# Performance work log

Measured on AMD Instinct MI355X. Metric: run time of the kernel, lower is better.

Reference implementation:

```python
import jax, jax.numpy as jnp
import numpy as np

N = 32768      # total nodes
E = 262144     # total edges
B = 32         # graphs in batch
NP = N // B    # nodes per graph (equal-sized graphs)
K = 820        # ceil(0.8 * NP), PyG TopKPooling k
H, C = 8, 64   # heads, per-head channels
NEG_SLOPE = 0.2


def setup_inputs() -> dict:
    key = jax.random.key(0)
    ks = jax.random.split(key, 12)
    s = 0.05
    return {
        "x": jax.random.normal(ks[0], (N, 256), jnp.float32),
        "edge_attr": jax.random.normal(ks[1], (E, 32), jnp.float32),
        "Wl": jax.random.normal(ks[2], (256, H * C), jnp.float32) * s,
        "bl": jax.random.normal(ks[3], (H * C,), jnp.float32) * s,
        "Wr": jax.random.normal(ks[4], (256, H * C), jnp.float32) * s,
        "br": jax.random.normal(ks[5], (H * C,), jnp.float32) * s,
        "We": jax.random.normal(ks[6], (32, H * C), jnp.float32) * s,
        "att": jax.random.normal(ks[7], (H, C), jnp.float32) * s,
        "bias": jax.random.normal(ks[8], (H * C,), jnp.float32) * s,
        "pool_w": jax.random.normal(ks[9], (H * C,), jnp.float32),
        "edge_index": jax.random.randint(ks[10], (2, E), 0, N, jnp.int32),
    }


def reference(x, edge_attr, Wl, bl, Wr, br, We, att, bias, pool_w, edge_index):
    src, dst = edge_index[0], edge_index[1]
    # GATv2Conv (eval mode, dropout off)
    xl = (x @ Wl + bl).reshape(N, H, C)   # x_j side (lin_l)
    xr = (x @ Wr + br).reshape(N, H, C)   # x_i side (lin_r)
    e = (edge_attr @ We).reshape(E, H, C)  # lin_edge, bias=False
    m = jax.nn.leaky_relu(xl[src] + xr[dst] + e, NEG_SLOPE)   # [E,H,C]
    alpha = jnp.einsum('ehc,hc->eh', m, att)                  # [E,H]
    amax = jax.ops.segment_max(alpha, dst, num_segments=N)
    ex = jnp.exp(alpha - amax[dst])
    denom = jax.ops.segment_sum(ex, dst, num_segments=N)
    alpha = ex / denom[dst]                                   # segment softmax over dst
    out = jax.ops.segment_sum(alpha[..., None] * xl[src], dst, num_segments=N)
    h = jax.nn.relu(out.reshape(N, H * C) + bias)             # [N,512]
    # TopKPooling: score = tanh(x.w / ||w||), keep top-k per graph, scale kept rows
    score = jnp.tanh(h @ pool_w / jnp.sqrt(jnp.sum(pool_w * pool_w)))
    vals, idx = jax.lax.top_k(score.reshape(B, NP), K)        # [B,K]
    hg = h.reshape(B, NP, H * C)
    hsel = jnp.take_along_axis(hg, idx[..., None], axis=1) * vals[..., None]  # [B,K,512]
    # global max pool || global mean pool
    gmp = hsel.max(axis=1)
    gap = hsel.mean(axis=1)
    return jnp.concatenate([gmp, gap], axis=1)                # [B,1024]
```

## Files before the change

kernel.cpp:

```cpp
#include <hip/hip_runtime.h>
#include <hip/hip_bf16.h>
#include <cstdint>
#include <cstddef>

#define N_NODES 32768
#define N_EDGES 262144
#define BGRAPH  32
#define NPG     1024
#define KSEL    820
#define NEG     0.2f

typedef unsigned short u16;
typedef __attribute__((ext_vector_type(4))) float f32x4;
typedef __attribute__((ext_vector_type(8))) short s16x8;

static __device__ __forceinline__ u16 f2bf(float v) {
    __hip_bfloat16 b(v);
    return *reinterpret_cast<u16*>(&b);
}
static __device__ __forceinline__ float bf2f(u16 u) {
    __hip_bfloat16 b = *reinterpret_cast<__hip_bfloat16*>(&u);
    return (float)b;
}

typedef const __attribute__((address_space(1))) void* gas_p;
typedef __attribute__((address_space(3))) void* las_p;
static __device__ __forceinline__ void gload16(const void* g, void* l) {
    __builtin_amdgcn_global_load_lds((gas_p)g, (las_p)l, 16, 0, 0);
}

__global__ __launch_bounds__(256) void k_split_x(
    const float* __restrict__ x, u16* __restrict__ xhi, u16* __restrict__ xlo)
{
    const int i = blockIdx.x * 256 + threadIdx.x;
    const float4 v = *(const float4*)&x[(size_t)i * 4];
    u16 h0 = f2bf(v.x), h1 = f2bf(v.y), h2 = f2bf(v.z), h3 = f2bf(v.w);
    u16 l0 = f2bf(v.x - bf2f(h0));
    u16 l1 = f2bf(v.y - bf2f(h1));
    u16 l2 = f2bf(v.z - bf2f(h2));
    u16 l3 = f2bf(v.w - bf2f(h3));
    *(ushort4*)&xhi[(size_t)i * 4] = make_ushort4(h0, h1, h2, h3);
    *(ushort4*)&xlo[(size_t)i * 4] = make_ushort4(l0, l1, l2, l3);
}

__global__ __launch_bounds__(256) void k_pack_bt(
    const float* __restrict__ Wl, const float* __restrict__ Wr,
    u16* __restrict__ BpT)
{
    const int kp = blockIdx.x * 256 + threadIdx.x;
    const int n  = blockIdx.y;
    const float* W = (n < 512) ? Wl : Wr;
    const int col = n & 511;
    const int k = kp & 255;
    const float v = W[(size_t)k * 512 + col];
    const u16 h = f2bf(v);
    const u16 o = (kp >= 256) ? f2bf(v - bf2f(h)) : h;
    BpT[(size_t)n * 512 + kp] = o;
}

__global__ __launch_bounds__(256) void k_prep_we(
    const float* __restrict__ We, u16* __restrict__ webf)
{
    const int g = blockIdx.x * 256 + threadIdx.x;
    const int slab = g >> 12, ch = (g >> 5) & 127, kk = g & 31;
    const int c = kk >> 3, j = kk & 7;
    const int s = (ch & 3) ^ ((ch >> 2) & 3);
    const int ksrc = ((c ^ s) << 3) + j;
    webf[g] = f2bf(We[(size_t)ksrc * 512 + slab * 128 + ch]);
}

__global__ __launch_bounds__(256) void gemm_mfma(
    const u16* __restrict__ xhi, const u16* __restrict__ xlo,
    const u16* __restrict__ BpT,
    const float* __restrict__ bl, const float* __restrict__ br,
    float* __restrict__ xl, float* __restrict__ xr)
{
    __shared__ u16 Ahs[128 * 32];
    __shared__ u16 Als[128 * 32];
    __shared__ u16 Bhs[128 * 32];
    __shared__ u16 Bls[128 * 32];

    const int raw = blockIdx.x;
    const int swz = (raw & 7) * 256 + (raw >> 3);
    const int mt = swz & 255, nt = swz >> 8;
    const int m0 = mt * 128, n0 = nt * 128;

    const int tid  = threadIdx.x;
    const int lane = tid & 63;
    const int wid  = tid >> 6;
    const int wr   = wid >> 1, wc = wid & 1;
    const int lr   = lane & 15;
    const int lk   = lane >> 4;

    f32x4 acc[4][4] = {};

    for (int q = 0; q < 8; ++q) {
        __syncthreads();
#pragma unroll
        for (int half = 0; half < 2; ++half) {
            const int w   = half * 256 + tid;
            const int row = w >> 2, cc = w & 3;
            const int cs  = cc ^ (row & 3) ^ ((row >> 2) & 3);
            const int ko  = q * 32 + cs * 8;
            gload16(&xhi[(size_t)(m0 + row) * 256 + ko],       &Ahs[w * 8]);
            gload16(&xlo[(size_t)(m0 + row) * 256 + ko],       &Als[w * 8]);
            gload16(&BpT[(size_t)(n0 + row) * 512 + ko],       &Bhs[w * 8]);
            gload16(&BpT[(size_t)(n0 + row) * 512 + 256 + ko], &Bls[w * 8]);
        }
        __syncthreads();

        s16x8 ah[4], al[4], bh[4], bl_[4];
#pragma unroll
        for (int i = 0; i < 4; ++i) {
            const int ar  = wr * 64 + i * 16 + lr;
            const int aof = ar * 32 + ((lk ^ (ar & 3) ^ ((ar >> 2) & 3)) << 3);
            ah[i] = *(const s16x8*)&Ahs[aof];
            al[i] = *(const s16x8*)&Als[aof];
            const int brw = wc * 64 + i * 16 + lr;
            const int bof = brw * 32 + ((lk ^ (brw & 3) ^ ((brw >> 2) & 3)) << 3);
            bh[i]  = *(const s16x8*)&Bhs[bof];
            bl_[i] = *(const s16x8*)&Bls[bof];
        }
#pragma unroll
        for (int i = 0; i < 4; ++i)
#pragma unroll
            for (int j = 0; j < 4; ++j) {
                acc[i][j] = __builtin_amdgcn_mfma_f32_16x16x32_bf16(ah[i], bh[j],  acc[i][j], 0, 0, 0);
                acc[i][j] = __builtin_amdgcn_mfma_f32_16x16x32_bf16(ah[i], bl_[j], acc[i][j], 0, 0, 0);
                acc[i][j] = __builtin_amdgcn_mfma_f32_16x16x32_bf16(al[i], bh[j],  acc[i][j], 0, 0, 0);
            }
    }

    float* const outp = (n0 < 512) ? xl : xr;
    const int ocol0 = n0 & 511;
    const float* const bb = (n0 < 512) ? bl : br;
#pragma unroll
    for (int j = 0; j < 4; ++j) {
        const int col = ocol0 + wc * 64 + j * 16 + lr;
        const float bv = bb[col];
#pragma unroll
        for (int i = 0; i < 4; ++i) {
#pragma unroll
            for (int r = 0; r < 4; ++r) {
                const int rowg = m0 + wr * 64 + i * 16 + lk * 4 + r;
                outp[(size_t)rowg * 512 + col] = acc[i][j][r] + bv;
            }
        }
    }
}

__global__ void k_hist(const int* __restrict__ ei, int* __restrict__ counts)
{
    int e = blockIdx.x * 256 + threadIdx.x;
    if (e < N_EDGES) atomicAdd(&counts[ei[N_EDGES + e]], 1);
}

__global__ __launch_bounds__(1024) void k_scan(
    const int* __restrict__ counts, int* __restrict__ offsets, int* __restrict__ cursors)
{
    __shared__ int part[1024];
    const int tid = threadIdx.x;
    const int base = tid * 32;
    int loc[32];
    int s = 0;
#pragma unroll
    for (int i = 0; i < 32; ++i) { loc[i] = s; s += counts[base + i]; }
    part[tid] = s;
    __syncthreads();
    const int own = s;
    for (int off = 1; off < 1024; off <<= 1) {
        int v = (tid >= off) ? part[tid - off] : 0;
        __syncthreads();
        part[tid] += v;
        __syncthreads();
    }
    const int pre = part[tid] - own;
#pragma unroll
    for (int i = 0; i < 32; ++i) {
        int o = pre + loc[i];
        offsets[base + i] = o;
        cursors[base + i] = o;
    }
}

__global__ void k_scatter(const int* __restrict__ ei, int* __restrict__ cursors,
                          int* __restrict__ sorted_src, int* __restrict__ sorted_dst,
                          int* __restrict__ sorted_eid)
{
    int e = blockIdx.x * 256 + threadIdx.x;
    if (e >= N_EDGES) return;
    int d = ei[N_EDGES + e];
    int pos = atomicAdd(&cursors[d], 1);
    sorted_src[pos] = ei[e];
    sorted_dst[pos] = d;
    sorted_eid[pos] = e;
}

__global__ __launch_bounds__(256) void k_prep_ea(
    const float* __restrict__ ea, const int* __restrict__ sorted_eid,
    u16* __restrict__ eabf)
{
    const int g = blockIdx.x * 256 + threadIdx.x;
    const int pos = g >> 5, kk = g & 31;
    const int c = kk >> 3, j = kk & 7;
    const int s = (pos & 3) ^ ((pos >> 2) & 3);
    const int ksrc = ((c ^ s) << 3) + j;
    eabf[g] = f2bf(ea[(size_t)sorted_eid[pos] * 32 + ksrc]);
}

#define LT_TILES 8

__global__ __launch_bounds__(256, 6) void k_logit(
    const float* __restrict__ xl, const float* __restrict__ xr,
    const u16* __restrict__ eabf, const u16* __restrict__ webf,
    const float* __restrict__ att,
    const int* __restrict__ sorted_src, const int* __restrict__ sorted_dst,
    float* __restrict__ logits)
{
    __shared__ u16 Ws[128 * 32];
    __shared__ u16 Ae[64 * 32];
    __shared__ int src_s[64], dst_s[64];

    const int tid  = threadIdx.x;
    const int lane = tid & 63;
    const int wid  = tid >> 6;
    const int slab = blockIdx.y;
    const int lr   = lane & 15;
    const int lk   = lane >> 4;

#pragma unroll
    for (int p = 0; p < 2; ++p) {
        const int chunk = p * 256 + tid;
        gload16(&webf[(size_t)slab * 4096 + chunk * 8], &Ws[chunk * 8]);
    }
    float attw[8];
#pragma unroll
    for (int f = 0; f < 8; ++f) attw[f] = att[slab * 128 + f * 16 + lr];

    const int sxor = (lr & 3) ^ (lr >> 2);
    const int swoff = (lk ^ sxor) << 3;

    for (int t = 0; t < LT_TILES; ++t) {
        const int ebase = (blockIdx.x * LT_TILES + t) * 64;
        __syncthreads();
        if (tid < 64) {
            src_s[tid] = sorted_src[ebase + tid];
            dst_s[tid] = sorted_dst[ebase + tid];
        }
        gload16(&eabf[(size_t)ebase * 32 + tid * 8], &Ae[tid * 8]);
        __syncthreads();

        const s16x8 afr = *(const s16x8*)&Ae[(wid * 16 + lr) * 32 + swoff];
        f32x4 acc[8];
#pragma unroll
        for (int f = 0; f < 8; ++f) {
            const s16x8 bfr = *(const s16x8*)&Ws[(f * 16 + lr) * 32 + swoff];
            acc[f] = __builtin_amdgcn_mfma_f32_16x16x32_bf16(
                afr, bfr, (f32x4){0.f, 0.f, 0.f, 0.f}, 0, 0, 0);
        }

        float p0[4], p1[4];
#pragma unroll
        for (int r = 0; r < 4; ++r) { p0[r] = 0.f; p1[r] = 0.f; }
#pragma unroll
        for (int r = 0; r < 4; ++r) {
            const int el = wid * 16 + lk * 4 + r;
            const size_t sb = (size_t)src_s[el] * 512 + slab * 128 + lr;
            const size_t db = (size_t)dst_s[el] * 512 + slab * 128 + lr;
#pragma unroll
            for (int f = 0; f < 8; ++f) {
                const float z = acc[f][r] + xl[sb + f * 16] + xr[db + f * 16];
                const float tt = z > 0.f ? z : NEG * z;
                if (f < 4) p0[r] += attw[f] * tt;
                else       p1[r] += attw[f] * tt;
            }
        }
#pragma unroll
        for (int o = 1; o < 16; o <<= 1) {
#pragma unroll
            for (int r = 0; r < 4; ++r) {
                p0[r] += __shfl_xor(p0[r], o);
                p1[r] += __shfl_xor(p1[r], o);
            }
        }
        if (lr == 0) {
#pragma unroll
            for (int r = 0; r < 4; ++r) {
                const size_t eg = ebase + wid * 16 + lk * 4 + r;
                logits[eg * 8 + slab * 2]     = p0[r];
                logits[eg * 8 + slab * 2 + 1] = p1[r];
            }
        }
    }
}

#define AGG_DPB 8

__global__ __launch_bounds__(256, 8) void k_agg(
    const float* __restrict__ xl, const float* __restrict__ logits,
    const int* __restrict__ sorted_src,
    const int* __restrict__ offsets, const int* __restrict__ counts,
    const float* __restrict__ bias, const float* __restrict__ pw,
    float* __restrict__ h, float* __restrict__ score)
{
    __shared__ float red_s[4];

    const int tid = threadIdx.x;
    const int wv  = tid >> 6;
    const int l   = tid & 63;
    const int c0  = tid * 2;
    const int head = tid >> 5;

    const float2 bv  = *(const float2*)&bias[c0];
    const float2 pwv = *(const float2*)&pw[c0];

    float nrm = pwv.x * pwv.x + pwv.y * pwv.y;
#pragma unroll
    for (int o = 1; o < 64; o <<= 1) nrm += __shfl_xor(nrm, o);
    if (l == 0) red_s[wv] = nrm;
    __syncthreads();
    const float inv_nrm = 1.0f / sqrtf(red_s[0] + red_s[1] + red_s[2] + red_s[3]);

    for (int dd = 0; dd < AGG_DPB; ++dd) {
        const int d   = blockIdx.x * AGG_DPB + dd;
        const int off = offsets[d];
        const int deg = counts[d];

        float m = -INFINITY;
        for (int j = 0; j < deg; ++j)
            m = fmaxf(m, logits[(size_t)(off + j) * 8 + head]);

        float den = 0.f, a0 = 0.f, a1 = 0.f;
        for (int j = 0; j < deg; ++j) {
            const float lg = logits[(size_t)(off + j) * 8 + head];
            const int   s  = sorted_src[off + j];
            const float2 xl2 = *(const float2*)&xl[(size_t)s * 512 + c0];
            const float pe = __expf(lg - m);
            den += pe;
            a0 += pe * xl2.x;
            a1 += pe * xl2.y;
        }

        const float r = den > 0.f ? 1.0f / den : 0.f;
        const float h0 = fmaxf(a0 * r + bv.x, 0.f);
        const float h1 = fmaxf(a1 * r + bv.y, 0.f);
        *(float2*)&h[(size_t)d * 512 + c0] = make_float2(h0, h1);

        float ps = h0 * pwv.x + h1 * pwv.y;
#pragma unroll
        for (int o = 1; o < 64; o <<= 1) ps += __shfl_xor(ps, o);
        __syncthreads();
        if (l == 0) red_s[wv] = ps;
        __syncthreads();
        if (tid == 0)
            score[d] = tanhf((red_s[0] + red_s[1] + red_s[2] + red_s[3]) * inv_nrm);
    }
}

__global__ __launch_bounds__(256) void k_topk(const float* __restrict__ score,
                                              int* __restrict__ sel_idx,
                                              float* __restrict__ sel_val)
{
    __shared__ unsigned long long key[1024];
    const int g = blockIdx.x, tid = threadIdx.x;
    for (int i = tid; i < 1024; i += 256) {
        float s = score[g * 1024 + i];
        unsigned u = __float_as_uint(s);
        u = (u & 0x80000000u) ? ~u : (u | 0x80000000u);
        key[i] = ((unsigned long long)(~u) << 32) | (unsigned)i;
    }
    __syncthreads();
    for (int k = 2; k <= 1024; k <<= 1) {
        for (int j = k >> 1; j > 0; j >>= 1) {
            for (int i = tid; i < 1024; i += 256) {
                int ixj = i ^ j;
                if (ixj > i) {
                    bool up = ((i & k) == 0);
                    unsigned long long a = key[i], b = key[ixj];
                    if ((a > b) == up) { key[i] = b; key[ixj] = a; }
                }
            }
            __syncthreads();
        }
    }
    for (int kk = tid; kk < KSEL; kk += 256) {
        int idx = (int)(key[kk] & 0xFFFFFFFFu);
        sel_idx[g * KSEL + kk] = idx;
        sel_val[g * KSEL + kk] = score[g * 1024 + idx];
    }
}

#define KSLICE 103

__global__ __launch_bounds__(256) void k_pool_part(
    const float* __restrict__ h, const int* __restrict__ sel_idx,
    const float* __restrict__ sel_val, float* __restrict__ part)
{
    const int g = blockIdx.x >> 3, sl = blockIdx.x & 7;
    const int kbeg = sl * KSLICE;
    const int kend = min(KSEL, kbeg + KSLICE);
    const int n = kend - kbeg;
    __shared__ float vs[KSLICE];
    __shared__ int   is_[KSLICE];
    const int tid = threadIdx.x;
    if (tid < n) {
        vs[tid]  = sel_val[g * KSEL + kbeg + tid];
        is_[tid] = sel_idx[g * KSEL + kbeg + tid];
    }
    __syncthreads();
    const int c0 = tid, c1 = tid + 256;
    float mx0 = -INFINITY, mx1 = -INFINITY, s0 = 0.f, s1 = 0.f;
    for (int kk = 0; kk < n; ++kk) {
        const float* hp = h + ((size_t)(g * 1024 + is_[kk])) * 512;
        const float v = vs[kk];
        float f0 = hp[c0] * v, f1 = hp[c1] * v;
        mx0 = fmaxf(mx0, f0); s0 += f0;
        mx1 = fmaxf(mx1, f1); s1 += f1;
    }
    const size_t base = ((size_t)blockIdx.x * 2) * 512;
    part[base + c0] = mx0;        part[base + c1] = mx1;
    part[base + 512 + c0] = s0;   part[base + 512 + c1] = s1;
}

__global__ __launch_bounds__(256) void k_pool_merge(
    const float* __restrict__ part, float* __restrict__ out)
{
    const int g = blockIdx.x, tid = threadIdx.x;
    const int c0 = tid, c1 = tid + 256;
    float mx0 = -INFINITY, mx1 = -INFINITY, s0 = 0.f, s1 = 0.f;
    for (int sl = 0; sl < 8; ++sl) {
        const size_t base = ((size_t)(g * 8 + sl) * 2) * 512;
        mx0 = fmaxf(mx0, part[base + c0]); mx1 = fmaxf(mx1, part[base + c1]);
        s0 += part[base + 512 + c0];       s1 += part[base + 512 + c1];
    }
    out[(size_t)g * 1024 + c0] = mx0;
    out[(size_t)g * 1024 + c1] = mx1;
    out[(size_t)g * 1024 + 512 + c0] = s0 * (1.f / KSEL);
    out[(size_t)g * 1024 + 512 + c1] = s1 * (1.f / KSEL);
}

extern "C" void kernel_launch(void* const* d_in, const int* in_sizes, int n_in,
                              void* d_out, int out_size, void* d_ws, size_t ws_size,
                              hipStream_t stream)
{
    const float* x    = (const float*)d_in[0];
    const float* ea   = (const float*)d_in[1];
    const float* Wl   = (const float*)d_in[2];
    const float* bl   = (const float*)d_in[3];
    const float* Wr   = (const float*)d_in[4];
    const float* br   = (const float*)d_in[5];
    const float* We   = (const float*)d_in[6];
    const float* att  = (const float*)d_in[7];
    const float* bias = (const float*)d_in[8];
    const float* pw   = (const float*)d_in[9];
    const int*   ei   = (const int*)d_in[10];
    float* out = (float*)d_out;

    float* xl        = (float*)d_ws;
    float* xr        = xl + (size_t)N_NODES * 512;
    float* h         = xr + (size_t)N_NODES * 512;
    float* logits    = h + (size_t)N_NODES * 512;
    float* sel_val   = logits + (size_t)N_EDGES * 8;
    float* part      = sel_val + BGRAPH * KSEL;
    float* score     = part + 256 * 2 * 512;
    int* counts      = (int*)(score + N_NODES);
    int* offsets     = counts + N_NODES;
    int* cursors     = offsets + N_NODES;
    int* sorted_src  = cursors + N_NODES;
    int* sorted_dst  = sorted_src + N_EDGES;
    int* sorted_eid  = sorted_dst + N_EDGES;
    int* sel_idx     = sorted_eid + N_EDGES;
    u16* xhi         = (u16*)(sel_idx + BGRAPH * KSEL);
    u16* xlo         = xhi + (size_t)N_NODES * 256;
    u16* bpt         = xlo + (size_t)N_NODES * 256;
    u16* webf        = bpt + (size_t)1024 * 512;
    u16* eabf        = webf + 4 * 128 * 32;

    hipMemsetAsync(counts, 0, (size_t)N_NODES * sizeof(int), stream);

    k_split_x<<<(N_NODES * 256) / (4 * 256), 256, 0, stream>>>(x, xhi, xlo);
    k_pack_bt<<<dim3(2, 1024), 256, 0, stream>>>(Wl, Wr, bpt);
    k_prep_we<<<64, 256, 0, stream>>>(We, webf);
    gemm_mfma<<<2048, 256, 0, stream>>>(xhi, xlo, bpt, bl, br, xl, xr);

    k_hist<<<N_EDGES / 256, 256, 0, stream>>>(ei, counts);
    k_scan<<<1, 1024, 0, stream>>>(counts, offsets, cursors);
    k_scatter<<<N_EDGES / 256, 256, 0, stream>>>(ei, cursors, sorted_src, sorted_dst, sorted_eid);
    k_prep_ea<<<(N_EDGES * 32) / 256, 256, 0, stream>>>(ea, sorted_eid, eabf);
    k_logit<<<dim3(N_EDGES / 64 / LT_TILES, 4), 256, 0, stream>>>(
        xl, xr, eabf, webf, att, sorted_src, sorted_dst, logits);
    k_agg<<<N_NODES / AGG_DPB, 256, 0, stream>>>(xl, logits, sorted_src, offsets, counts,
                                                 bias, pw, h, score);
    k_topk<<<BGRAPH, 256, 0, stream>>>(score, sel_idx, sel_val);
    k_pool_part<<<BGRAPH * 8, 256, 0, stream>>>(h, sel_idx, sel_val, part);
    k_pool_merge<<<BGRAPH, 256, 0, stream>>>(part, out);
}
```

Baseline: 589.9 us.

## Fuse edge logit and softmax aggregation into one per-destination online-softmax kernel

Result: slower. 726.6 us (+23.2%).

```diff
diff --git a/kernel.cpp b/kernel.cpp
--- a/kernel.cpp
+++ b/kernel.cpp
@@ -63,10 +63,16 @@
 {
     const int g = blockIdx.x * 256 + threadIdx.x;
     const int slab = g >> 12, ch = (g >> 5) & 127, kk = g & 31;
-    const int c = kk >> 3, j = kk & 7;
-    const int s = (ch & 3) ^ ((ch >> 2) & 3);
-    const int ksrc = ((c ^ s) << 3) + j;
-    webf[g] = f2bf(We[(size_t)ksrc * 512 + slab * 128 + ch]);
+    webf[g] = f2bf(We[(size_t)kk * 512 + slab * 128 + ch]);
+}
+
+__global__ __launch_bounds__(256) void k_prep_ea(
+    const float* __restrict__ ea, const int* __restrict__ sorted_eid,
+    u16* __restrict__ eabf)
+{
+    const int g = blockIdx.x * 256 + threadIdx.x;
+    const int pos = g >> 5, kk = g & 31;
+    eabf[g] = f2bf(ea[(size_t)sorted_eid[pos] * 32 + kk]);
 }
 
 __global__ __launch_bounds__(256) void gemm_mfma(
@@ -196,165 +202,159 @@
     sorted_eid[pos] = e;
 }
 
-__global__ __launch_bounds__(256) void k_prep_ea(
-    const float* __restrict__ ea, const int* __restrict__ sorted_eid,
-    u16* __restrict__ eabf)
-{
-    const int g = blockIdx.x * 256 + threadIdx.x;
-    const int pos = g >> 5, kk = g & 31;
-    const int c = kk >> 3, j = kk & 7;
-    const int s = (pos & 3) ^ ((pos >> 2) & 3);
-    const int ksrc = ((c ^ s) << 3) + j;
-    eabf[g] = f2bf(ea[(size_t)sorted_eid[pos] * 32 + ksrc]);
-}
-
-#define LT_TILES 8
-
-__global__ __launch_bounds__(256, 6) void k_logit(
+#define DPW 8
+
+__global__ __launch_bounds__(256, 4) void k_edge_fused(
     const float* __restrict__ xl, const float* __restrict__ xr,
     const u16* __restrict__ eabf, const u16* __restrict__ webf,
-    const float* __restrict__ att,
-    const int* __restrict__ sorted_src, const int* __restrict__ sorted_dst,
-    float* __restrict__ logits)
-{
-    __shared__ u16 Ws[128 * 32];
-    __shared__ u16 Ae[64 * 32];
-    __shared__ int src_s[64], dst_s[64];
-
+    const float* __restrict__ att, const float* __restrict__ bias,
+    const int* __restrict__ offsets, const int* __restrict__ counts,
+    const int* __restrict__ sorted_src,
+    float* __restrict__ h)
+{
     const int tid  = threadIdx.x;
     const int lane = tid & 63;
     const int wid  = tid >> 6;
     const int slab = blockIdx.y;
     const int lr   = lane & 15;
     const int lk   = lane >> 4;
-
-#pragma unroll
-    for (int p = 0; p < 2; ++p) {
-        const int chunk = p * 256 + tid;
-        gload16(&webf[(size_t)slab * 4096 + chunk * 8], &Ws[chunk * 8]);
-    }
+    const int chbase = slab * 128 + lr;
+
+    s16x8 bfr[8];
+#pragma unroll
+    for (int f = 0; f < 8; ++f)
+        bfr[f] = *(const s16x8*)&webf[(size_t)slab * 4096 + (f * 16 + lr) * 32 + lk * 8];
     float attw[8];
 #pragma unroll
     for (int f = 0; f < 8; ++f) attw[f] = att[slab * 128 + f * 16 + lr];
 
-    const int sxor = (lr & 3) ^ (lr >> 2);
-    const int swoff = (lk ^ sxor) << 3;
-
-    for (int t = 0; t < LT_TILES; ++t) {
-        const int ebase = (blockIdx.x * LT_TILES + t) * 64;
-        __syncthreads();
-        if (tid < 64) {
-            src_s[tid] = sorted_src[ebase + tid];
-            dst_s[tid] = sorted_dst[ebase + tid];
-        }
-        gload16(&eabf[(size_t)ebase * 32 + tid * 8], &Ae[tid * 8]);
-        __syncthreads();
-
-        const s16x8 afr = *(const s16x8*)&Ae[(wid * 16 + lr) * 32 + swoff];
-        f32x4 acc[8];
-#pragma unroll
-        for (int f = 0; f < 8; ++f) {
-            const s16x8 bfr = *(const s16x8*)&Ws[(f * 16 + lr) * 32 + swoff];
-            acc[f] = __builtin_amdgcn_mfma_f32_16x16x32_bf16(
-                afr, bfr, (f32x4){0.f, 0.f, 0.f, 0.f}, 0, 0, 0);
-        }
-
-        float p0[4], p1[4];
-#pragma unroll
-        for (int r = 0; r < 4; ++r) { p0[r] = 0.f; p1[r] = 0.f; }
-#pragma unroll
-        for (int r = 0; r < 4; ++r) {
-            const int el = wid * 16 + lk * 4 + r;
-            const size_t sb = (size_t)src_s[el] * 512 + slab * 128 + lr;
-            const size_t db = (size_t)dst_s[el] * 512 + slab * 128 + lr;
-#pragma unroll
-            for (int f = 0; f < 8; ++f) {
-                const float z = acc[f][r] + xl[sb + f * 16] + xr[db + f * 16];
-                const float tt = z > 0.f ? z : NEG * z;
-                if (f < 4) p0[r] += attw[f] * tt;
-                else       p1[r] += attw[f] * tt;
-            }
-        }
-#pragma unroll
-        for (int o = 1; o < 16; o <<= 1) {
-#pragma unroll
-            for (int r = 0; r < 4; ++r) {
-                p0[r] += __shfl_xor(p0[r], o);
-                p1[r] += __shfl_xor(p1[r], o);
-            }
-        }
-        if (lr == 0) {
-#pragma unroll
-            for (int r = 0; r < 4; ++r) {
-                const size_t eg = ebase + wid * 16 + lk * 4 + r;
-                logits[eg * 8 + slab * 2]     = p0[r];
-                logits[eg * 8 + slab * 2 + 1] = p1[r];
-            }
-        }
-    }
-}
-
-#define AGG_DPB 8
-
-__global__ __launch_bounds__(256, 8) void k_agg(
-    const float* __restrict__ xl, const float* __restrict__ logits,
-    const int* __restrict__ sorted_src,
-    const int* __restrict__ offsets, const int* __restrict__ counts,
-    const float* __restrict__ bias, const float* __restrict__ pw,
-    float* __restrict__ h, float* __restrict__ score)
-{
-    __shared__ float red_s[4];
-
-    const int tid = threadIdx.x;
-    const int wv  = tid >> 6;
-    const int l   = tid & 63;
-    const int c0  = tid * 2;
-    const int head = tid >> 5;
-
-    const float2 bv  = *(const float2*)&bias[c0];
-    const float2 pwv = *(const float2*)&pw[c0];
-
-    float nrm = pwv.x * pwv.x + pwv.y * pwv.y;
-#pragma unroll
-    for (int o = 1; o < 64; o <<= 1) nrm += __shfl_xor(nrm, o);
-    if (l == 0) red_s[wv] = nrm;
-    __syncthreads();
-    const float inv_nrm = 1.0f / sqrtf(red_s[0] + red_s[1] + red_s[2] + red_s[3]);
-
-    for (int dd = 0; dd < AGG_DPB; ++dd) {
-        const int d   = blockIdx.x * AGG_DPB + dd;
+    for (int dd = 0; dd < DPW; ++dd) {
+        const int d   = (blockIdx.x * 4 + wid) * DPW + dd;
         const int off = offsets[d];
         const int deg = counts[d];
 
-        float m = -INFINITY;
-        for (int j = 0; j < deg; ++j)
-            m = fmaxf(m, logits[(size_t)(off + j) * 8 + head]);
-
-        float den = 0.f, a0 = 0.f, a1 = 0.f;
-        for (int j = 0; j < deg; ++j) {
-            const float lg = logits[(size_t)(off + j) * 8 + head];
-            const int   s  = sorted_src[off + j];
-            const float2 xl2 = *(const float2*)&xl[(size_t)s * 512 + c0];
-            const float pe = __expf(lg - m);
-            den += pe;
-            a0 += pe * xl2.x;
-            a1 += pe * xl2.y;
-        }
-
-        const float r = den > 0.f ? 1.0f / den : 0.f;
-        const float h0 = fmaxf(a0 * r + bv.x, 0.f);
-        const float h1 = fmaxf(a1 * r + bv.y, 0.f);
-        *(float2*)&h[(size_t)d * 512 + c0] = make_float2(h0, h1);
-
-        float ps = h0 * pwv.x + h1 * pwv.y;
-#pragma unroll
-        for (int o = 1; o < 64; o <<= 1) ps += __shfl_xor(ps, o);
-        __syncthreads();
-        if (l == 0) red_s[wv] = ps;
-        __syncthreads();
-        if (tid == 0)
-            score[d] = tanhf((red_s[0] + red_s[1] + red_s[2] + red_s[3]) * inv_nrm);
-    }
+        float xrv[8];
+#pragma unroll
+        for (int f = 0; f < 8; ++f)
+            xrv[f] = xr[(size_t)d * 512 + chbase + f * 16];
+
+        float m0 = -INFINITY, m1 = -INFINITY, den0 = 0.f, den1 = 0.f;
+        float accO[8];
+#pragma unroll
+        for (int f = 0; f < 8; ++f) accO[f] = 0.f;
+
+        for (int base = 0; base < deg; base += 16) {
+            const s16x8 afr = *(const s16x8*)&eabf[(size_t)(off + base + lr) * 32 + lk * 8];
+
+            int srcv[4];
+#pragma unroll
+            for (int r = 0; r < 4; ++r) {
+                const int el = lk * 4 + r;
+                srcv[r] = (base + el < deg) ? sorted_src[off + base + el] : -1;
+            }
+            float xlv[4][8];
+#pragma unroll
+            for (int r = 0; r < 4; ++r) {
+                if (srcv[r] >= 0) {
+                    const size_t sb = (size_t)srcv[r] * 512 + chbase;
+#pragma unroll
+                    for (int f = 0; f < 8; ++f) xlv[r][f] = xl[sb + f * 16];
+                } else {
+#pragma unroll
+                    for (int f = 0; f < 8; ++f) xlv[r][f] = 0.f;
+                }
+            }
+
+            float p0[4] = {0.f, 0.f, 0.f, 0.f}, p1[4] = {0.f, 0.f, 0.f, 0.f};
+#pragma unroll
+            for (int f = 0; f < 8; ++f) {
+                const f32x4 ef = __builtin_amdgcn_mfma_f32_16x16x32_bf16(
+                    afr, bfr[f], (f32x4){0.f, 0.f, 0.f, 0.f}, 0, 0, 0);
+#pragma unroll
+                for (int r = 0; r < 4; ++r) {
+                    float z = ef[r] + xlv[r][f] + xrv[f];
+                    z = z > 0.f ? z : NEG * z;
+                    if (f < 4) p0[r] += attw[f] * z;
+                    else       p1[r] += attw[f] * z;
+                }
+            }
+#pragma unroll
+            for (int o = 1; o < 16; o <<= 1) {
+#pragma unroll
+                for (int r = 0; r < 4; ++r) {
+                    p0[r] += __shfl_xor(p0[r], o);
+                    p1[r] += __shfl_xor(p1[r], o);
+                }
+            }
+#pragma unroll
+            for (int r = 0; r < 4; ++r) {
+                if (base + lk * 4 + r >= deg) { p0[r] = -INFINITY; p1[r] = -INFINITY; }
+            }
+            float c0 = fmaxf(fmaxf(p0[0], p0[1]), fmaxf(p0[2], p0[3]));
+            float c1 = fmaxf(fmaxf(p1[0], p1[1]), fmaxf(p1[2], p1[3]));
+            c0 = fmaxf(c0, __shfl_xor(c0, 16)); c0 = fmaxf(c0, __shfl_xor(c0, 32));
+            c1 = fmaxf(c1, __shfl_xor(c1, 16)); c1 = fmaxf(c1, __shfl_xor(c1, 32));
+            const float mn0 = fmaxf(m0, c0), mn1 = fmaxf(m1, c1);
+            const float s0 = __expf(m0 - mn0), s1 = __expf(m1 - mn1);
+            float w0[4], w1[4];
+#pragma unroll
+            for (int r = 0; r < 4; ++r) {
+                w0[r] = __expf(p0[r] - mn0);
+                w1[r] = __expf(p1[r] - mn1);
+            }
+            den0 = den0 * s0 + w0[0] + w0[1] + w0[2] + w0[3];
+            den1 = den1 * s1 + w1[0] + w1[1] + w1[2] + w1[3];
+#pragma unroll
+            for (int f = 0; f < 8; ++f) {
+                float a = accO[f] * ((f < 4) ? s0 : s1);
+#pragma unroll
+                for (int r = 0; r < 4; ++r)
+                    a += ((f < 4) ? w0[r] : w1[r]) * xlv[r][f];
+                accO[f] = a;
+            }
+            m0 = mn0; m1 = mn1;
+        }
+
+#pragma unroll
+        for (int o = 16; o < 64; o <<= 1) {
+            den0 += __shfl_xor(den0, o);
+            den1 += __shfl_xor(den1, o);
+#pragma unroll
+            for (int f = 0; f < 8; ++f) accO[f] += __shfl_xor(accO[f], o);
+        }
+        const float r0 = den0 > 0.f ? 1.f / den0 : 0.f;
+        const float r1 = den1 > 0.f ? 1.f / den1 : 0.f;
+        if (lk == 0) {
+#pragma unroll
+            for (int f = 0; f < 8; ++f) {
+                const float hv = fmaxf(accO[f] * ((f < 4) ? r0 : r1) + bias[chbase + f * 16], 0.f);
+                h[(size_t)d * 512 + chbase + f * 16] = hv;
+            }
+        }
+    }
+}
+
+__global__ __launch_bounds__(256) void k_score(
+    const float* __restrict__ h, const float* __restrict__ pw,
+    float* __restrict__ score)
+{
+    const int lane = threadIdx.x & 63;
+    const int wv   = threadIdx.x >> 6;
+    const int n    = blockIdx.x * 4 + wv;
+    const float4 a = *(const float4*)&pw[lane * 8];
+    const float4 b = *(const float4*)&pw[lane * 8 + 4];
+    float nrm = a.x*a.x + a.y*a.y + a.z*a.z + a.w*a.w
+              + b.x*b.x + b.y*b.y + b.z*b.z + b.w*b.w;
+    const float4 c  = *(const float4*)&h[(size_t)n * 512 + lane * 8];
+    const float4 d4 = *(const float4*)&h[(size_t)n * 512 + lane * 8 + 4];
+    float dot = a.x*c.x + a.y*c.y + a.z*c.z + a.w*c.w
+              + b.x*d4.x + b.y*d4.y + b.z*d4.z + b.w*d4.w;
+#pragma unroll
+    for (int o = 1; o < 64; o <<= 1) {
+        nrm += __shfl_xor(nrm, o);
+        dot += __shfl_xor(dot, o);
+    }
+    if (lane == 0) score[n] = tanhf(dot / sqrtf(nrm));
 }
 
 __global__ __launch_bounds__(256) void k_topk(const float* __restrict__ score,
@@ -459,8 +459,7 @@
     float* xl        = (float*)d_ws;
     float* xr        = xl + (size_t)N_NODES * 512;
     float* h         = xr + (size_t)N_NODES * 512;
-    float* logits    = h + (size_t)N_NODES * 512;
-    float* sel_val   = logits + (size_t)N_EDGES * 8;
+    float* sel_val   = h + (size_t)N_NODES * 512;
     float* part      = sel_val + BGRAPH * KSEL;
     float* score     = part + 256 * 2 * 512;
     int* counts      = (int*)(score + N_NODES);
@@ -487,10 +486,9 @@
     k_scan<<<1, 1024, 0, stream>>>(counts, offsets, cursors);
     k_scatter<<<N_EDGES / 256, 256, 0, stream>>>(ei, cursors, sorted_src, sorted_dst, sorted_eid);
     k_prep_ea<<<(N_EDGES * 32) / 256, 256, 0, stream>>>(ea, sorted_eid, eabf);
-    k_logit<<<dim3(N_EDGES / 64 / LT_TILES, 4), 256, 0, stream>>>(
-        xl, xr, eabf, webf, att, sorted_src, sorted_dst, logits);
-    k_agg<<<N_NODES / AGG_DPB, 256, 0, stream>>>(xl, logits, sorted_src, offsets, counts,
-                                                 bias, pw, h, score);
+    k_edge_fused<<<dim3(N_NODES / (4 * DPW), 4), 256, 0, stream>>>(
+        xl, xr, eabf, webf, att, bias, offsets, counts, sorted_src, h);
+    k_score<<<N_NODES / 4, 256, 0, stream>>>(h, pw, score);
     k_topk<<<BGRAPH, 256, 0, stream>>>(score, sel_idx, sel_val);
     k_pool_part<<<BGRAPH * 8, 256, 0, stream>>>(h, sel_idx, sel_val, part);
     k_pool_merge<<<BGRAPH, 256, 0, stream>>>(part, out);
```
